# Performance work log

Hardware: AMD Instinct MI355X
Metric: run time of the kernel (lower is better)

## Reference

```python
import jax, jax.numpy as jnp
import numpy as np

NB = 4
QN = -(2 ** (NB - 1))   # -8
QP = 2 ** (NB - 1) - 1  # 7
EPS = 1e-5


def _grad_scale(x, g):
    # forward: x, backward: grad * g (LSQ gradient scaling)
    return x * g + jax.lax.stop_gradient(x - x * g)


def _round_pass(x):
    # round with straight-through estimator
    return x + jax.lax.stop_gradient(jnp.round(x) - x)


def _lsq(v, alpha, qn, qp):
    # LSQ fake quantize-dequantize with learnable step size alpha
    g = 1.0 / np.sqrt(v.size * qp)
    a = _grad_scale(alpha, g)
    return _round_pass(jnp.clip(v / a, qn, qp)) * a


def _bn(x, g, b, m, v):
    # eval-mode BatchNorm2d over channel dim of NCHW
    s = (g * jax.lax.rsqrt(v + EPS))[None, :, None, None]
    return (x - m[None, :, None, None]) * s + b[None, :, None, None]


def _conv(x, w, stride, pad, groups):
    return jax.lax.conv_general_dilated(
        x, w, (stride, stride), pad,
        dimension_numbers=('NCHW', 'OIHW', 'NCHW'),
        feature_group_count=groups)


def setup_inputs() -> dict:
    key = jax.random.key(0)
    ks = jax.random.split(key, 4)
    inp, oup, hid = 96, 96, 576
    B, H, W = 32, 28, 28
    d = {}
    d['x'] = jax.random.normal(ks[0], (B, inp, H, W), jnp.float32)
    d['w1'] = jax.random.normal(ks[1], (hid, inp, 1, 1), jnp.float32) * 0.1
    d['w2'] = jax.random.normal(ks[2], (hid, 1, 3, 3), jnp.float32) * 0.1
    d['w3'] = jax.random.normal(ks[3], (oup, hid, 1, 1), jnp.float32) * 0.1
    for i, c in zip((1, 2, 3), (hid, hid, oup)):
        d[f'aw{i}'] = jnp.full((1,), 0.05, jnp.float32)  # weight step size
        d[f'ax{i}'] = jnp.full((1,), 0.5, jnp.float32)   # activation step size
        d[f'g{i}'] = jnp.ones((c,), jnp.float32)
        d[f'b{i}'] = jnp.zeros((c,), jnp.float32)
        d[f'm{i}'] = jnp.zeros((c,), jnp.float32)
        d[f'v{i}'] = jnp.ones((c,), jnp.float32)
    return d


def reference(x, w1, w2, w3, aw1, ax1, g1, b1, m1, v1,
              aw2, ax2, g2, b2, m2, v2, aw3, ax3, g3, b3, m3, v3):
    hid = w1.shape[0]
    # 1x1 expand conv (LSQ on activation and weight)
    h = _conv(_lsq(x, ax1, QN, QP), _lsq(w1, aw1, QN, QP), 1, [(0, 0), (0, 0)], 1)
    h = jnp.clip(_bn(h, g1, b1, m1, v1), 0.0, 6.0)
    # 3x3 depthwise conv, stride 1
    h = _conv(_lsq(h, ax2, QN, QP), _lsq(w2, aw2, QN, QP), 1, [(1, 1), (1, 1)], hid)
    h = jnp.clip(_bn(h, g2, b2, m2, v2), 0.0, 6.0)
    # 1x1 project conv
    h = _conv(_lsq(h, ax3, QN, QP), _lsq(w3, aw3, QN, QP), 1, [(0, 0), (0, 0)], 1)
    h = _bn(h, g3, b3, m3, v3)
    # identity residual (stride==1 and inp==oup)
    return x + h
```

## Files before the change

### kernel.cpp

```cpp
#include <hip/hip_runtime.h>

#define EPSF 1e-5f

typedef int    int4v   __attribute__((ext_vector_type(4)));
typedef float  float4v __attribute__((ext_vector_type(4)));

#define W1P_OFF  0
#define W3P_OFF  55296
#define W2QI_OFF 110592
#define S1B1_OFF 115776
#define S2B2_OFF 120384
#define S3B3_OFF 124992

#define H1S 296
#define H2S 600

__device__ __forceinline__ float lsq_q(float v, float a) {
    float t = v / a;
    t = fminf(fmaxf(t, -8.0f), 7.0f);
    return rintf(t);
}

__device__ __forceinline__ long q8pack_w(const float* s, float a) {
    unsigned long long v = 0;
    #pragma unroll
    for (int j = 0; j < 8; ++j) {
        int q = (int)lsq_q(s[j], a);
        v |= (unsigned long long)(q & 255) << (8 * j);
    }
    return (long)v;
}

__global__ __launch_bounds__(256)
void prep_w(const float* __restrict__ w1, const float* __restrict__ w2,
            const float* __restrict__ w3,
            const float* aw1, const float* ax1, const float* ax2,
            const float* aw2, const float* ax3, const float* aw3,
            const float* __restrict__ g1, const float* __restrict__ b1,
            const float* __restrict__ m1, const float* __restrict__ v1,
            const float* __restrict__ g2, const float* __restrict__ b2,
            const float* __restrict__ m2, const float* __restrict__ v2,
            const float* __restrict__ g3, const float* __restrict__ b3,
            const float* __restrict__ m3, const float* __restrict__ v3,
            long* __restrict__ w1p, long* __restrict__ w3p,
            signed char* __restrict__ w2qi,
            float* __restrict__ s1b1, float* __restrict__ s2b2,
            float* __restrict__ s3b3) {
    int id = blockIdx.x * 256 + threadIdx.x;
    if (id < 6912) {
        int l = id & 63, t = id >> 6;
        int kc = t % 3, ct = t / 3;
        int co = ct * 16 + (l & 15);
        int ci0 = kc * 32 + (l >> 4) * 8;
        w1p[id] = q8pack_w(w1 + co * 96 + ci0, aw1[0]);
    } else if (id < 13824) {
        int i = id - 6912;
        int l = i & 63, t = i >> 6;
        int kc = t % 18, ct = t / 18;
        int co = ct * 16 + (l & 15);
        int ci0 = kc * 32 + (l >> 4) * 8;
        w3p[i] = q8pack_w(w3 + co * 576 + ci0, aw3[0]);
    } else if (id < 19008) {
        int i = id - 13824;
        int c = i % 576, tap = i / 576;
        w2qi[i] = (signed char)(int)lsq_q(w2[c * 9 + tap], aw2[0]);
    } else if (id < 19584) {
        int c = id - 19008;
        float s = g1[c] / sqrtf(v1[c] + EPSF);
        float A = aw1[0] * ax1[0];
        float inv = 1.0f / ax2[0];
        s1b1[c] = A * s * inv;
        s1b1[576 + c] = (b1[c] - m1[c] * s) * inv;
    } else if (id < 20160) {
        int c = id - 19584;
        float s = g2[c] / sqrtf(v2[c] + EPSF);
        float A = ax2[0] * aw2[0];
        float inv = 1.0f / ax3[0];
        s2b2[c] = A * s * inv;
        s2b2[576 + c] = (b2[c] - m2[c] * s) * inv;
    } else if (id < 20256) {
        int c = id - 20160;
        float s = g3[c] / sqrtf(v3[c] + EPSF);
        float A = ax3[0] * aw3[0];
        s3b3[c] = A * s;
        s3b3[96 + c] = b3[c] - m3[c] * s;
    }
}

__global__ __launch_bounds__(448, 4)
void fused_k(const float* __restrict__ x, const long* __restrict__ w1p,
             const signed char* __restrict__ w2qi, const long* __restrict__ w3p,
             const float* __restrict__ ax1,
             const float* __restrict__ s1b1, const float* __restrict__ s2b2,
             const float* __restrict__ s3b3, float* __restrict__ out) {
    __shared__ __align__(16) signed char h1[112 * H1S];
    __shared__ __align__(16) signed char h2[64 * H2S];
    const int tid = threadIdx.x;
    const int w = tid >> 6, l = tid & 63;
    const int quad = l >> 4, c16 = l & 15;
    const int b = blockIdx.x;
    const int r0 = blockIdx.y * 2;

    {
        const int lp = w * 16 + c16;
        int row = r0 - 1 + lp / 28;
        row = min(max(row, 0), 27);
        const int p = row * 28 + lp % 28;
        const float inv1 = 1.0f / ax1[0];

        long bfr[3];
        #pragma unroll
        for (int kc = 0; kc < 3; ++kc) {
            const float* xs = x + (b * 96 + kc * 32 + quad * 8) * 784 + p;
            unsigned long long v = 0;
            #pragma unroll
            for (int j = 0; j < 8; ++j) {
                float t = xs[j * 784] * inv1;
                t = fminf(fmaxf(t, -8.0f), 7.0f);
                int q = (int)rintf(t);
                v |= (unsigned long long)(q & 255) << (8 * j);
            }
            bfr[kc] = (long)v;
        }
        #pragma unroll 4
        for (int ct = 0; ct < 36; ++ct) {
            int4v acc; acc[0] = 0; acc[1] = 0; acc[2] = 0; acc[3] = 0;
            #pragma unroll
            for (int kc = 0; kc < 3; ++kc)
                acc = __builtin_amdgcn_mfma_i32_16x16x32_i8(
                    w1p[(ct * 3 + kc) * 64 + l], bfr[kc], acc, 0, 0, 0);
            const int co0 = ct * 16 + quad * 4;
            float4v S = *(const float4v*)(s1b1 + co0);
            float4v B = *(const float4v*)(s1b1 + 576 + co0);
            int pk = 0;
            #pragma unroll
            for (int r = 0; r < 4; ++r) {
                float t = fmaf((float)acc[r], S[r], B[r]);
                t = fminf(fmaxf(t, 0.0f), 7.0f);
                pk |= ((int)rintf(t)) << (4 * r);
            }
            *(unsigned short*)(h1 + lp * H1S + (co0 >> 1)) = (unsigned short)pk;
        }
    }
    __syncthreads();

    #pragma unroll
    for (int i = 0; i < 9; ++i) {
        const int idx = tid + 448 * i;
        const int pos = idx / 72, g = idx - (idx / 72) * 72;
        const int row_in = pos / 28, col = pos - (pos / 28) * 28;
        int acc[8] = {0, 0, 0, 0, 0, 0, 0, 0};
        #pragma unroll
        for (int dh = -1; dh <= 1; ++dh) {
            if ((unsigned)(r0 + row_in + dh) >= 28u) continue;
            #pragma unroll
            for (int dc = -1; dc <= 1; ++dc) {
                if ((unsigned)(col + dc) >= 28u) continue;
                const int lp = (row_in + 1 + dh) * 28 + col + dc;
                const unsigned int xv = *(const unsigned int*)(h1 + lp * H1S + g * 4);
                const int tap = (dh + 1) * 3 + dc + 1;
                const int w0  = *(const int*)(w2qi + tap * 576 + g * 8);
                const int w1v = *(const int*)(w2qi + tap * 576 + g * 8 + 4);
                #pragma unroll
                for (int j = 0; j < 4; ++j) {
                    acc[j]     += (int)((xv >> (4 * j)) & 15u)       * ((w0  << (24 - 8 * j)) >> 24);
                    acc[4 + j] += (int)((xv >> (4 * (4 + j))) & 15u) * ((w1v << (24 - 8 * j)) >> 24);
                }
            }
        }
        int pk0 = 0, pk1 = 0;
        #pragma unroll
        for (int j = 0; j < 8; ++j) {
            const int c = g * 8 + j;
            float t = fmaf((float)acc[j], s2b2[c], s2b2[576 + c]);
            t = fminf(fmaxf(t, 0.0f), 7.0f);
            const int q = (int)rintf(t);
            if (j < 4) pk0 |= q << (8 * j); else pk1 |= q << (8 * (j - 4));
        }
        int2 pk; pk.x = pk0; pk.y = pk1;
        *(int2*)(h2 + pos * H2S + g * 8) = pk;
    }
    __syncthreads();

    for (int t = w; t < 24; t += 7) {
        const int nt = t / 6, ct = t - (t / 6) * 6;
        int4v acc; acc[0] = 0; acc[1] = 0; acc[2] = 0; acc[3] = 0;
        const signed char* arow = h2 + (nt * 16 + c16) * H2S + quad * 8;
        #pragma unroll 6
        for (int kc = 0; kc < 18; ++kc)
            acc = __builtin_amdgcn_mfma_i32_16x16x32_i8(
                *(const long*)(arow + kc * 32),
                w3p[(ct * 18 + kc) * 64 + l], acc, 0, 0, 0);
        const int nloc = nt * 16 + quad * 4;
        if (nloc < 56) {
            const int co = ct * 16 + c16;
            const float S = s3b3[co], Bv = s3b3[96 + co];
            const int off = (b * 96 + co) * 784 + r0 * 28 + nloc;
            const float4v xr = *(const float4v*)(x + off);
            float4v o;
            #pragma unroll
            for (int r = 0; r < 4; ++r)
                o[r] = fmaf((float)acc[r], S, Bv) + xr[r];
            *(float4v*)(out + off) = o;
        }
    }
}

extern "C" void kernel_launch(void* const* d_in, const int* in_sizes, int n_in,
                              void* d_out, int out_size, void* d_ws, size_t ws_size,
                              hipStream_t stream) {
    const float* x   = (const float*)d_in[0];
    const float* w1  = (const float*)d_in[1];
    const float* w2  = (const float*)d_in[2];
    const float* w3  = (const float*)d_in[3];
    const float* aw1 = (const float*)d_in[4];
    const float* ax1 = (const float*)d_in[5];
    const float* g1  = (const float*)d_in[6];
    const float* b1  = (const float*)d_in[7];
    const float* m1  = (const float*)d_in[8];
    const float* v1  = (const float*)d_in[9];
    const float* aw2 = (const float*)d_in[10];
    const float* ax2 = (const float*)d_in[11];
    const float* g2  = (const float*)d_in[12];
    const float* b2  = (const float*)d_in[13];
    const float* m2  = (const float*)d_in[14];
    const float* v2  = (const float*)d_in[15];
    const float* aw3 = (const float*)d_in[16];
    const float* ax3 = (const float*)d_in[17];
    const float* g3  = (const float*)d_in[18];
    const float* b3  = (const float*)d_in[19];
    const float* m3  = (const float*)d_in[20];
    const float* v3  = (const float*)d_in[21];

    char* ws = (char*)d_ws;
    long* w1p = (long*)(ws + W1P_OFF);
    long* w3p = (long*)(ws + W3P_OFF);
    signed char* w2qi = (signed char*)(ws + W2QI_OFF);
    float* s1b1 = (float*)(ws + S1B1_OFF);
    float* s2b2 = (float*)(ws + S2B2_OFF);
    float* s3b3 = (float*)(ws + S3B3_OFF);

    float* out = (float*)d_out;

    prep_w<<<80, 256, 0, stream>>>(w1, w2, w3, aw1, ax1, ax2, aw2, ax3, aw3,
                                   g1, b1, m1, v1, g2, b2, m2, v2, g3, b3, m3, v3,
                                   w1p, w3p, w2qi, s1b1, s2b2, s3b3);
    dim3 grid(32, 14);
    fused_k<<<grid, 448, 0, stream>>>(x, w1p, w2qi, w3p, ax1, s1b1, s2b2, s3b3, out);
}
```

Baseline: 151.8 us.

## Compute depthwise 3x3 conv with int8 MFMA using block-diagonal weight matrices

Replaces the scalar nibble-unpack multiply-accumulate depthwise stage with int8 MFMA instructions. The prep kernel builds block-diagonal weight fragments, with two taps per k-chunk and five k-chunks covering nine taps. The h1 shared buffer becomes zero-padded (30-wide rows, 120 positions) so boundary checks vanish. This adds about 8x redundant MACs from the mostly-zero block-diagonal weights, a shared-memory clearing pass, and a larger weight workspace read from global memory.

```diff
diff --git a/kernel.cpp b/kernel.cpp
--- a/kernel.cpp
+++ b/kernel.cpp
@@ -7,10 +7,10 @@
 
 #define W1P_OFF  0
 #define W3P_OFF  55296
-#define W2QI_OFF 110592
-#define S1B1_OFF 115776
-#define S2B2_OFF 120384
-#define S3B3_OFF 124992
+#define W2D_OFF  110592
+#define S1B1_OFF 202752
+#define S2B2_OFF 207360
+#define S3B3_OFF 211968
 
 #define H1S 296
 #define H2S 600
@@ -21,11 +21,11 @@
     return rintf(t);
 }
 
-__device__ __forceinline__ long q8pack_w(const float* s, float a) {
+__device__ __forceinline__ long q8pack_w(const float* w, int base, const int* idx, float a) {
     unsigned long long v = 0;
     #pragma unroll
     for (int j = 0; j < 8; ++j) {
-        int q = (int)lsq_q(s[j], a);
+        int q = (int)lsq_q(w[base + idx[j]], a);
         v |= (unsigned long long)(q & 255) << (8 * j);
     }
     return (long)v;
@@ -43,43 +43,56 @@
             const float* __restrict__ g3, const float* __restrict__ b3,
             const float* __restrict__ m3, const float* __restrict__ v3,
             long* __restrict__ w1p, long* __restrict__ w3p,
-            signed char* __restrict__ w2qi,
+            long* __restrict__ w2d,
             float* __restrict__ s1b1, float* __restrict__ s2b2,
             float* __restrict__ s3b3) {
     int id = blockIdx.x * 256 + threadIdx.x;
+    const int lin[8] = {0, 1, 2, 3, 4, 5, 6, 7};
     if (id < 6912) {
         int l = id & 63, t = id >> 6;
         int kc = t % 3, ct = t / 3;
         int co = ct * 16 + (l & 15);
         int ci0 = kc * 32 + (l >> 4) * 8;
-        w1p[id] = q8pack_w(w1 + co * 96 + ci0, aw1[0]);
+        w1p[id] = q8pack_w(w1, co * 96 + ci0, lin, aw1[0]);
     } else if (id < 13824) {
         int i = id - 6912;
         int l = i & 63, t = i >> 6;
         int kc = t % 18, ct = t / 18;
         int co = ct * 16 + (l & 15);
         int ci0 = kc * 32 + (l >> 4) * 8;
-        w3p[i] = q8pack_w(w3 + co * 576 + ci0, aw3[0]);
-    } else if (id < 19008) {
+        w3p[i] = q8pack_w(w3, co * 576 + ci0, lin, aw3[0]);
+    } else if (id < 25344) {
         int i = id - 13824;
-        int c = i % 576, tap = i / 576;
-        w2qi[i] = (signed char)(int)lsq_q(w2[c * 9 + tap], aw2[0]);
-    } else if (id < 19584) {
-        int c = id - 19008;
+        int l = i & 63, t = i >> 6;
+        int kc = t % 5, ct = t / 5;
+        int quad = l >> 4, m = l & 15;
+        int tap = kc * 2 + (quad >> 1);
+        unsigned long long v = 0;
+        if (tap <= 8) {
+            int mh = m - (quad & 1) * 8;
+            if (mh >= 0 && mh < 8) {
+                int j = (mh >> 1) | ((mh & 1) << 2);
+                int q = (int)lsq_q(w2[(ct * 16 + m) * 9 + tap], aw2[0]);
+                v = (unsigned long long)(unsigned)(q & 255) << (8 * j);
+            }
+        }
+        w2d[i] = (long)v;
+    } else if (id < 25920) {
+        int c = id - 25344;
         float s = g1[c] / sqrtf(v1[c] + EPSF);
         float A = aw1[0] * ax1[0];
         float inv = 1.0f / ax2[0];
         s1b1[c] = A * s * inv;
         s1b1[576 + c] = (b1[c] - m1[c] * s) * inv;
-    } else if (id < 20160) {
-        int c = id - 19584;
+    } else if (id < 26496) {
+        int c = id - 25920;
         float s = g2[c] / sqrtf(v2[c] + EPSF);
         float A = ax2[0] * aw2[0];
         float inv = 1.0f / ax3[0];
         s2b2[c] = A * s * inv;
         s2b2[576 + c] = (b2[c] - m2[c] * s) * inv;
-    } else if (id < 20256) {
-        int c = id - 20160;
+    } else if (id < 26592) {
+        int c = id - 26496;
         float s = g3[c] / sqrtf(v3[c] + EPSF);
         float A = ax3[0] * aw3[0];
         s3b3[c] = A * s;
@@ -89,23 +102,29 @@
 
 __global__ __launch_bounds__(448, 4)
 void fused_k(const float* __restrict__ x, const long* __restrict__ w1p,
-             const signed char* __restrict__ w2qi, const long* __restrict__ w3p,
+             const long* __restrict__ w2d, const long* __restrict__ w3p,
              const float* __restrict__ ax1,
              const float* __restrict__ s1b1, const float* __restrict__ s2b2,
              const float* __restrict__ s3b3, float* __restrict__ out) {
-    __shared__ __align__(16) signed char h1[112 * H1S];
+    __shared__ __align__(16) signed char h1[120 * H1S];
     __shared__ __align__(16) signed char h2[64 * H2S];
     const int tid = threadIdx.x;
     const int w = tid >> 6, l = tid & 63;
     const int quad = l >> 4, c16 = l & 15;
+    const int qh = quad >> 1, ql = quad & 1;
     const int b = blockIdx.x;
     const int r0 = blockIdx.y * 2;
 
+    for (int i = tid; i < 120 * H1S / 16; i += 448)
+        ((int4v*)h1)[i] = (int4v){0, 0, 0, 0};
+    __syncthreads();
+
     {
         const int lp = w * 16 + c16;
-        int row = r0 - 1 + lp / 28;
-        row = min(max(row, 0), 27);
-        const int p = row * 28 + lp % 28;
+        const int row = lp / 28, col = lp - (lp / 28) * 28;
+        const int img_row = r0 - 1 + row;
+        const bool valid = (unsigned)img_row < 28u;
+        const int p = min(max(img_row, 0), 27) * 28 + col;
         const float inv1 = 1.0f / ax1[0];
 
         long bfr[3];
@@ -122,6 +141,7 @@
             }
             bfr[kc] = (long)v;
         }
+        const int pos_h = row * 30 + col + 1;
         #pragma unroll 4
         for (int ct = 0; ct < 36; ++ct) {
             int4v acc; acc[0] = 0; acc[1] = 0; acc[2] = 0; acc[3] = 0;
@@ -139,46 +159,45 @@
                 t = fminf(fmaxf(t, 0.0f), 7.0f);
                 pk |= ((int)rintf(t)) << (4 * r);
             }
-            *(unsigned short*)(h1 + lp * H1S + (co0 >> 1)) = (unsigned short)pk;
+            if (valid)
+                *(unsigned short*)(h1 + pos_h * H1S + (co0 >> 1)) = (unsigned short)pk;
         }
     }
     __syncthreads();
 
-    #pragma unroll
-    for (int i = 0; i < 9; ++i) {
-        const int idx = tid + 448 * i;
-        const int pos = idx / 72, g = idx - (idx / 72) * 72;
-        const int row_in = pos / 28, col = pos - (pos / 28) * 28;
-        int acc[8] = {0, 0, 0, 0, 0, 0, 0, 0};
+    for (int t = w; t < 144; t += 7) {
+        const int pt = t / 36, ct = t - (t / 36) * 36;
+        const int pos = pt * 16 + c16;
+        const int posc = min(pos, 55);
+        const int row_in = posc / 28, col = posc - (posc / 28) * 28;
+        const int choff = ct * 8 + ql * 4;
+        int4v acc; acc[0] = 0; acc[1] = 0; acc[2] = 0; acc[3] = 0;
         #pragma unroll
-        for (int dh = -1; dh <= 1; ++dh) {
-            if ((unsigned)(r0 + row_in + dh) >= 28u) continue;
-            #pragma unroll
-            for (int dc = -1; dc <= 1; ++dc) {
-                if ((unsigned)(col + dc) >= 28u) continue;
-                const int lp = (row_in + 1 + dh) * 28 + col + dc;
-                const unsigned int xv = *(const unsigned int*)(h1 + lp * H1S + g * 4);
-                const int tap = (dh + 1) * 3 + dc + 1;
-                const int w0  = *(const int*)(w2qi + tap * 576 + g * 8);
-                const int w1v = *(const int*)(w2qi + tap * 576 + g * 8 + 4);
-                #pragma unroll
-                for (int j = 0; j < 4; ++j) {
-                    acc[j]     += (int)((xv >> (4 * j)) & 15u)       * ((w0  << (24 - 8 * j)) >> 24);
-                    acc[4 + j] += (int)((xv >> (4 * (4 + j))) & 15u) * ((w1v << (24 - 8 * j)) >> 24);
-                }
-            }
-        }
-        int pk0 = 0, pk1 = 0;
-        #pragma unroll
-        for (int j = 0; j < 8; ++j) {
-            const int c = g * 8 + j;
-            float t = fmaf((float)acc[j], s2b2[c], s2b2[576 + c]);
-            t = fminf(fmaxf(t, 0.0f), 7.0f);
-            const int q = (int)rintf(t);
-            if (j < 4) pk0 |= q << (8 * j); else pk1 |= q << (8 * (j - 4));
-        }
-        int2 pk; pk.x = pk0; pk.y = pk1;
-        *(int2*)(h2 + pos * H2S + g * 8) = pk;
+        for (int kc = 0; kc < 5; ++kc) {
+            int tap = kc * 2 + qh;
+            tap = min(tap, 8);
+            const int dh = tap / 3 - 1, dc = tap - (tap / 3) * 3 - 1;
+            const int pos_h = (row_in + 1 + dh) * 30 + (col + 1 + dc);
+            const unsigned v = *(const unsigned*)(h1 + pos_h * H1S + choff);
+            const unsigned lo = v & 0x0F0F0F0Fu;
+            const unsigned hi = (v >> 4) & 0x0F0F0F0Fu;
+            const long bf = (long)(((unsigned long long)hi << 32) | lo);
+            acc = __builtin_amdgcn_mfma_i32_16x16x32_i8(
+                w2d[(ct * 5 + kc) * 64 + l], bf, acc, 0, 0, 0);
+        }
+        if (pos < 56) {
+            const int c0 = ct * 16 + quad * 4;
+            float4v S = *(const float4v*)(s2b2 + c0);
+            float4v B = *(const float4v*)(s2b2 + 576 + c0);
+            int pk = 0;
+            #pragma unroll
+            for (int r = 0; r < 4; ++r) {
+                float tt = fmaf((float)acc[r], S[r], B[r]);
+                tt = fminf(fmaxf(tt, 0.0f), 7.0f);
+                pk |= ((int)rintf(tt)) << (8 * r);
+            }
+            *(int*)(h2 + pos * H2S + c0) = pk;
+        }
     }
     __syncthreads();
 
@@ -235,16 +254,16 @@
     char* ws = (char*)d_ws;
     long* w1p = (long*)(ws + W1P_OFF);
     long* w3p = (long*)(ws + W3P_OFF);
-    signed char* w2qi = (signed char*)(ws + W2QI_OFF);
+    long* w2d = (long*)(ws + W2D_OFF);
     float* s1b1 = (float*)(ws + S1B1_OFF);
     float* s2b2 = (float*)(ws + S2B2_OFF);
     float* s3b3 = (float*)(ws + S3B3_OFF);
 
     float* out = (float*)d_out;
 
-    prep_w<<<80, 256, 0, stream>>>(w1, w2, w3, aw1, ax1, ax2, aw2, ax3, aw3,
-                                   g1, b1, m1, v1, g2, b2, m2, v2, g3, b3, m3, v3,
-                                   w1p, w3p, w2qi, s1b1, s2b2, s3b3);
+    prep_w<<<104, 256, 0, stream>>>(w1, w2, w3, aw1, ax1, ax2, aw2, ax3, aw3,
+                                    g1, b1, m1, v1, g2, b2, m2, v2, g3, b3, m3, v3,
+                                    w1p, w3p, w2d, s1b1, s2b2, s3b3);
     dim3 grid(32, 14);
-    fused_k<<<grid, 448, 0, stream>>>(x, w1p, w2qi, w3p, ax1, s1b1, s2b2, s3b3, out);
-}
+    fused_k<<<grid, 448, 0, stream>>>(x, w1p, w2d, w3p, ax1, s1b1, s2b2, s3b3, out);
+}
```

Measured after the change: 145.0 us. -4.5%, faster.
